# Performance work log

Measured on AMD Instinct MI355X. Metric: run time of the kernel, lower is better.

Reference implementation:

```python
import jax, jax.numpy as jnp
import numpy as np


def _cell(x, h, c, Wih, Whh, bih, bhh):
    # PyTorch LSTM cell, gate order i, f, g, o
    g = x @ Wih.T + h @ Whh.T + bih + bhh
    i, f, gg, o = jnp.split(g, 4, axis=-1)
    c = jax.nn.sigmoid(f) * c + jax.nn.sigmoid(i) * jnp.tanh(gg)
    h = jax.nn.sigmoid(o) * jnp.tanh(c)
    return h, c


def _run_layer(x, Wih, Whh, bih, bhh):
    # x: (B, T, I) -> (hs (B,T,H), hT (B,H), cT (B,H))
    B = x.shape[0]
    H = Whh.shape[1]
    h0 = jnp.zeros((B, H), x.dtype)
    c0 = jnp.zeros((B, H), x.dtype)

    def step(carry, xt):
        h, c = carry
        h, c = _cell(xt, h, c, Wih, Whh, bih, bhh)
        return (h, c), h

    (hT, cT), hs = jax.lax.scan(step, (h0, c0), jnp.swapaxes(x, 0, 1))
    return jnp.swapaxes(hs, 0, 1), hT, cT


def setup_inputs() -> dict:
    key = jax.random.key(0)
    B, T_HIST, F, H, T_FUT = 16384, 20, 10, 128, 30
    s = 0.08  # ~1/sqrt(hidden) init scale
    ks = jax.random.split(key, 20)
    inp = {
        'hist':   jax.random.normal(ks[0], (B, T_HIST, F), jnp.float32),
        'e_Wih0': jax.random.normal(ks[1], (4 * H, F), jnp.float32) * s,
        'e_Whh0': jax.random.normal(ks[2], (4 * H, H), jnp.float32) * s,
        'e_bih0': jax.random.normal(ks[3], (4 * H,), jnp.float32) * s,
        'e_bhh0': jax.random.normal(ks[4], (4 * H,), jnp.float32) * s,
        'e_Wih1': jax.random.normal(ks[5], (4 * H, H), jnp.float32) * s,
        'e_Whh1': jax.random.normal(ks[6], (4 * H, H), jnp.float32) * s,
        'e_bih1': jax.random.normal(ks[7], (4 * H,), jnp.float32) * s,
        'e_bhh1': jax.random.normal(ks[8], (4 * H,), jnp.float32) * s,
        'd_Wih0': jax.random.normal(ks[9], (4 * H, 2), jnp.float32) * s,
        'd_Whh0': jax.random.normal(ks[10], (4 * H, H), jnp.float32) * s,
        'd_bih0': jax.random.normal(ks[11], (4 * H,), jnp.float32) * s,
        'd_bhh0': jax.random.normal(ks[12], (4 * H,), jnp.float32) * s,
        'd_Wih1': jax.random.normal(ks[13], (4 * H, H), jnp.float32) * s,
        'd_Whh1': jax.random.normal(ks[14], (4 * H, H), jnp.float32) * s,
        'd_bih1': jax.random.normal(ks[15], (4 * H,), jnp.float32) * s,
        'd_bhh1': jax.random.normal(ks[16], (4 * H,), jnp.float32) * s,
        'head_W': jax.random.normal(ks[17], (2, H), jnp.float32) * s,
        'head_b': jax.random.normal(ks[18], (2,), jnp.float32) * s,
        'fut_len': T_FUT,
    }
    return inp


def reference(hist, e_Wih0, e_Whh0, e_bih0, e_bhh0, e_Wih1, e_Whh1, e_bih1, e_bhh1,
              d_Wih0, d_Whh0, d_bih0, d_bhh0, d_Wih1, d_Whh1, d_bih1, d_bhh1,
              head_W, head_b, fut_len):
    B = hist.shape[0]
    # 2-layer encoder over history
    h1, hT0, cT0 = _run_layer(hist, e_Wih0, e_Whh0, e_bih0, e_bhh0)
    _, hT1, cT1 = _run_layer(h1, e_Wih1, e_Whh1, e_bih1, e_bhh1)

    def step(carry, _):
        y, h0, c0, h1_, c1_ = carry
        nh0, nc0 = _cell(y, h0, c0, d_Wih0, d_Whh0, d_bih0, d_bhh0)
        nh1, nc1 = _cell(nh0, h1_, c1_, d_Wih1, d_Whh1, d_bih1, d_bhh1)
        dxy = nh1 @ head_W.T + head_b  # (B, 2)
        return (dxy, nh0, nc0, nh1, nc1), dxy

    y0 = jnp.zeros((B, 2), hist.dtype)
    _, ys = jax.lax.scan(step, (y0, hT0, cT0, hT1, cT1), None, length=fut_len)
    return jnp.swapaxes(ys, 0, 1)  # (B, fut_len, 2)
```

## Files before the change

### kernel.cpp

```cpp
#include <hip/hip_runtime.h>


typedef __attribute__((ext_vector_type(8))) short short8;
typedef __attribute__((ext_vector_type(4))) float float4v;

#define MFMA16(a, b, c) __builtin_amdgcn_mfma_f32_16x16x32_bf16((a), (b), (c), 0, 0, 0)

__device__ __forceinline__ unsigned short f2bf(float x) {
    unsigned u = __builtin_bit_cast(unsigned, x);
    unsigned r = (u + 0x7FFFu + ((u >> 16) & 1u)) >> 16;
    return (unsigned short)r;
}
__device__ __forceinline__ float bf2f(unsigned short b) {
    unsigned u = ((unsigned)b) << 16;
    return __builtin_bit_cast(float, u);
}

#if __has_builtin(__builtin_amdgcn_exp2f)
__device__ __forceinline__ float vexp2(float x) { return __builtin_amdgcn_exp2f(x); }
#else
__device__ __forceinline__ float vexp2(float x) { return exp2f(x); }
#endif
#if __has_builtin(__builtin_amdgcn_rcpf)
__device__ __forceinline__ float vrcp(float x) { return __builtin_amdgcn_rcpf(x); }
#else
__device__ __forceinline__ float vrcp(float x) { return 1.0f / x; }
#endif

__device__ __forceinline__ float sigm(float x) {
    return vrcp(1.0f + vexp2(x * -1.442695040888963f));
}
__device__ __forceinline__ float tanh_(float x) {
    return 1.0f - 2.0f * vrcp(1.0f + vexp2(x * 2.885390081777927f));
}

__global__ void prep_kernel(const float* __restrict__ eWih0, const float* __restrict__ eWhh0,
                            const float* __restrict__ ebih0, const float* __restrict__ ebhh0,
                            const float* __restrict__ eWih1, const float* __restrict__ eWhh1,
                            const float* __restrict__ ebih1, const float* __restrict__ ebhh1,
                            const float* __restrict__ dWih0, const float* __restrict__ dWhh0,
                            const float* __restrict__ dbih0, const float* __restrict__ dbhh0,
                            const float* __restrict__ dWih1, const float* __restrict__ dWhh1,
                            const float* __restrict__ dbih1, const float* __restrict__ dbhh1,
                            void* __restrict__ ws)
{
    int i = blockIdx.x * 256 + threadIdx.x;
    short* We0 = (short*)ws;
    short* We1 = We0 + 512 * 160;
    short* Wd0 = We1 + 512 * 256;
    short* Wd1 = Wd0 + 512 * 128;
    float* bsT = (float*)((char*)ws + 819200);
    float* wyT = bsT + 2048;
    const int N0 = 512 * 160, N1 = 512 * 256, N2 = 512 * 128, N3 = 512 * 256;
    if (i < N0) {
        int n = i / 160, k = i - n * 160;
        float v = (k < 32) ? (k < 10 ? eWih0[n * 10 + k] : 0.0f) : eWhh0[n * 128 + (k - 32)];
        We0[i] = (short)f2bf(v);
    } else if (i < N0 + N1) {
        int ii = i - N0, n = ii >> 8, k = ii & 255;
        float v = (k < 128) ? eWih1[n * 128 + k] : eWhh1[n * 128 + (k - 128)];
        We1[ii] = (short)f2bf(v);
    } else if (i < N0 + N1 + N2) {
        int ii = i - (N0 + N1);
        Wd0[ii] = (short)f2bf(dWhh0[ii]);
    } else if (i < N0 + N1 + N2 + N3) {
        int ii = i - (N0 + N1 + N2), n = ii >> 8, k = ii & 255;
        float v = (k < 128) ? dWih1[n * 128 + k] : dWhh1[n * 128 + (k - 128)];
        Wd1[ii] = (short)f2bf(v);
    } else if (i < N0 + N1 + N2 + N3 + 2048) {
        int ii = i - (N0 + N1 + N2 + N3);
        int set = ii >> 9, r = ii & 511, j = r >> 2, q = r & 3;
        int g = q * 128 + j;
        float v = (set == 0) ? ebih0[g] + ebhh0[g]
                : (set == 1) ? ebih1[g] + ebhh1[g]
                : (set == 2) ? dbih0[g] + dbhh0[g]
                             : dbih1[g] + dbhh1[g];
        bsT[ii] = v;
    } else if (i < N0 + N1 + N2 + N3 + 2048 + 1024) {
        int ii = i - (N0 + N1 + N2 + N3 + 2048);
        int j = ii >> 3, e = ii & 7, q = e >> 1, cc = e & 1;
        wyT[ii] = dWih0[(q * 128 + j) * 2 + cc];
    }
}


template <int NKT>
__device__ __forceinline__ void mma4(float4v acc[4][4], const short8* __restrict__ hb,
                                     const char* __restrict__ wb, const unsigned* wo,
                                     int woff, int nib, int quad)
{
#pragma unroll 1
    for (int kk = 0; kk < NKT; ++kk) {
        int sx = ((kk * 4 + quad) ^ nib) + nib * 16;
        short8 a0 = hb[sx];
        short8 a1 = hb[256 + sx];
        short8 a2 = hb[512 + sx];
        short8 a3 = hb[768 + sx];
        short8 b0 = *(const short8*)(wb + (wo[0] + woff + kk * 64));
        short8 b1 = *(const short8*)(wb + (wo[1] + woff + kk * 64));
        short8 b2 = *(const short8*)(wb + (wo[2] + woff + kk * 64));
        short8 b3 = *(const short8*)(wb + (wo[3] + woff + kk * 64));
        acc[0][0] = MFMA16(a0, b0, acc[0][0]);
        acc[0][1] = MFMA16(a1, b0, acc[0][1]);
        acc[0][2] = MFMA16(a2, b0, acc[0][2]);
        acc[0][3] = MFMA16(a3, b0, acc[0][3]);
        acc[1][0] = MFMA16(a0, b1, acc[1][0]);
        acc[1][1] = MFMA16(a1, b1, acc[1][1]);
        acc[1][2] = MFMA16(a2, b1, acc[1][2]);
        acc[1][3] = MFMA16(a3, b1, acc[1][3]);
        acc[2][0] = MFMA16(a0, b2, acc[2][0]);
        acc[2][1] = MFMA16(a1, b2, acc[2][1]);
        acc[2][2] = MFMA16(a2, b2, acc[2][2]);
        acc[2][3] = MFMA16(a3, b2, acc[2][3]);
        acc[3][0] = MFMA16(a0, b3, acc[3][0]);
        acc[3][1] = MFMA16(a1, b3, acc[3][1]);
        acc[3][2] = MFMA16(a2, b3, acc[3][2]);
        acc[3][3] = MFMA16(a3, b3, acc[3][3]);
    }
}

template <bool DEC0>
__device__ __forceinline__ void cell_update4(float4v acc[4][4], float4v bv,
                                             float* __restrict__ cbase,
                                             unsigned short* __restrict__ hdst,
                                             const float* __restrict__ ybuf,
                                             float4v wy0, float4v wy1,
                                             int j, int quad)
{
    int kc = j >> 3;
    int jl = j & 7;
#pragma unroll
    for (int mt = 0; mt < 4; ++mt) {
#pragma unroll
        for (int r = 0; r < 4; ++r) {
            float gi = acc[0][mt][r] + bv[0];
            float gf = acc[1][mt][r] + bv[1];
            float gg = acc[2][mt][r] + bv[2];
            float go = acc[3][mt][r] + bv[3];
            int m = mt * 16 + quad * 4 + r;
            if (DEC0) {
                float y0 = ybuf[2 * m], y1 = ybuf[2 * m + 1];
                gi += y0 * wy0[0] + y1 * wy0[1];
                gf += y0 * wy0[2] + y1 * wy0[3];
                gg += y0 * wy1[0] + y1 * wy1[1];
                go += y0 * wy1[2] + y1 * wy1[3];
            }
            float si = sigm(gi);
            float sf = sigm(gf);
            float tg = tanh_(gg);
            float so = sigm(go);
            float* cp = cbase + (m * 132 + j);
            float c = sf * (*cp) + si * tg;
            *cp = c;
            float h = so * tanh_(c);
            int slot = m * 16 + (kc ^ (m & 15));
            hdst[slot * 8 + jl] = f2bf(h);
        }
    }
}

__global__ void __attribute__((amdgpu_flat_work_group_size(512, 512), amdgpu_waves_per_eu(2)))
lstm_main(
    const float* __restrict__ hist,
    const float* __restrict__ headW, const float* __restrict__ headB,
    const int* __restrict__ futlen, const void* __restrict__ ws,
    float* __restrict__ out)
{
    __shared__ short8 h0buf[2][1024];
    __shared__ short8 h1buf[2][1024];
    __shared__ short8 xbuf[2][256];
    __shared__ float ybuf[128];
    __shared__ float cbuf0[64 * 132];
    __shared__ float cbuf1[64 * 132];

    const char* wsb = (const char*)ws;
    const char* We0 = wsb;
    const char* We1 = wsb + 512 * 160 * 2;
    const char* Wd0 = We1 + 512 * 256 * 2;
    const char* Wd1 = Wd0 + 512 * 128 * 2;
    const float* bsT = (const float*)(wsb + 819200);
    const float* wyT = bsT + 2048;

    const int tid = threadIdx.x;
    const int w = tid >> 6;
    const int lane = tid & 63;
    const int quad = lane >> 4;
    const int nib = lane & 15;
    const int b0 = blockIdx.x * 64;
    const int TFUT = *futlen;
    const int j = 16 * w + nib;

    h0buf[0][tid] = (short8)0;
    h0buf[0][512 + tid] = (short8)0;
    h1buf[0][tid] = (short8)0;
    h1buf[0][512 + tid] = (short8)0;
    h1buf[1][tid] = (short8)0;
    h1buf[1][512 + tid] = (short8)0;
    ((short8*)xbuf)[tid] = (short8)0;
    if (tid < 128) ybuf[tid] = 0.0f;
    for (int i = tid; i < 64 * 132; i += 512) {
        cbuf0[i] = 0.0f;
        cbuf1[i] = 0.0f;
    }
    __syncthreads();

    if (tid < 128) {
        int m = tid & 63, part = tid >> 6;
        const float* hp = hist + ((size_t)((b0 + m) * 20 + 0)) * 10;
        float v[8];
        if (part == 0) {
#pragma unroll
            for (int i = 0; i < 8; ++i) v[i] = hp[i];
        } else {
            v[0] = hp[8]; v[1] = hp[9];
#pragma unroll
            for (int i = 2; i < 8; ++i) v[i] = 0.0f;
        }
        short8 pk;
#pragma unroll
        for (int i = 0; i < 8; ++i) pk[i] = (short)f2bf(v[i]);
        xbuf[0][m * 4 + (part ^ (m & 3))] = pk;
    }

    unsigned eo0[4], eo1[4];
#pragma unroll
    for (int q = 0; q < 4; ++q) {
        unsigned row = 16u * (w + 8 * q) + nib;
        eo0[q] = row * 320u + quad * 16u;
        eo1[q] = row * 512u + quad * 16u;
    }
    int p0 = 0, p1 = 0, px = 0;
    __syncthreads();

#pragma unroll 1
    for (int wdw = 0; wdw < 21; ++wdw) {
        if (wdw < 20) {
            float4v acc[4][4];
#pragma unroll
            for (int q = 0; q < 4; ++q)
#pragma unroll
                for (int mt = 0; mt < 4; ++mt) acc[q][mt] = (float4v){0.f, 0.f, 0.f, 0.f};
            {
                const short8* xb = xbuf[px];
                int sxx = (quad ^ (nib & 3)) + nib * 4;
                short8 a0 = xb[sxx];
                short8 a1 = xb[64 + sxx];
                short8 a2 = xb[128 + sxx];
                short8 a3 = xb[192 + sxx];
                short8 bq0 = *(const short8*)(We0 + eo0[0]);
                short8 bq1 = *(const short8*)(We0 + eo0[1]);
                short8 bq2 = *(const short8*)(We0 + eo0[2]);
                short8 bq3 = *(const short8*)(We0 + eo0[3]);
                acc[0][0] = MFMA16(a0, bq0, acc[0][0]);
                acc[0][1] = MFMA16(a1, bq0, acc[0][1]);
                acc[0][2] = MFMA16(a2, bq0, acc[0][2]);
                acc[0][3] = MFMA16(a3, bq0, acc[0][3]);
                acc[1][0] = MFMA16(a0, bq1, acc[1][0]);
                acc[1][1] = MFMA16(a1, bq1, acc[1][1]);
                acc[1][2] = MFMA16(a2, bq1, acc[1][2]);
                acc[1][3] = MFMA16(a3, bq1, acc[1][3]);
                acc[2][0] = MFMA16(a0, bq2, acc[2][0]);
                acc[2][1] = MFMA16(a1, bq2, acc[2][1]);
                acc[2][2] = MFMA16(a2, bq2, acc[2][2]);
                acc[2][3] = MFMA16(a3, bq2, acc[2][3]);
                acc[3][0] = MFMA16(a0, bq3, acc[3][0]);
                acc[3][1] = MFMA16(a1, bq3, acc[3][1]);
                acc[3][2] = MFMA16(a2, bq3, acc[3][2]);
                acc[3][3] = MFMA16(a3, bq3, acc[3][3]);
            }
            mma4<4>(acc, h0buf[p0], We0, eo0, 64, nib, quad);
            float4v bv = *(const float4v*)(bsT + 0 * 512 + j * 4);
            cell_update4<false>(acc, bv, cbuf0, (unsigned short*)h0buf[p0 ^ 1], nullptr,
                                (float4v){0, 0, 0, 0}, (float4v){0, 0, 0, 0}, j, quad);
        }

        if (tid < 128 && wdw < 19) {
            int m = tid & 63, part = tid >> 6;
            const float* hp = hist + ((size_t)((b0 + m) * 20 + (wdw + 1))) * 10;
            float v[8];
            if (part == 0) {
#pragma unroll
                for (int i = 0; i < 8; ++i) v[i] = hp[i];
            } else {
                v[0] = hp[8]; v[1] = hp[9];
#pragma unroll
                for (int i = 2; i < 8; ++i) v[i] = 0.0f;
            }
            short8 pk;
#pragma unroll
            for (int i = 0; i < 8; ++i) pk[i] = (short)f2bf(v[i]);
            xbuf[px ^ 1][m * 4 + (part ^ (m & 3))] = pk;
        }

        if (wdw >= 1) {
            float4v acc[4][4];
#pragma unroll
            for (int q = 0; q < 4; ++q)
#pragma unroll
                for (int mt = 0; mt < 4; ++mt) acc[q][mt] = (float4v){0.f, 0.f, 0.f, 0.f};
            mma4<4>(acc, h0buf[p0], We1, eo1, 0, nib, quad);
            mma4<4>(acc, h1buf[p1], We1, eo1, 256, nib, quad);
            float4v bv = *(const float4v*)(bsT + 1 * 512 + j * 4);
            cell_update4<false>(acc, bv, cbuf1, (unsigned short*)h1buf[p1 ^ 1], nullptr,
                                (float4v){0, 0, 0, 0}, (float4v){0, 0, 0, 0}, j, quad);
        }
        __syncthreads();
        p0 ^= 1; p1 ^= 1; px ^= 1;
    }

    p0 = 0;
    p1 = 1;

    unsigned do0[4];
#pragma unroll
    for (int q = 0; q < 4; ++q) {
        unsigned row = 16u * (w + 8 * q) + nib;
        do0[q] = row * 256u + quad * 16u;
    }

#pragma unroll 1
    for (int t = 0; t < TFUT; ++t) {
        if (tid < 128 && t >= 1) {
            int m = tid & 63, jj = tid >> 6;
            const short8* hb = h1buf[p1];
            const float4v* hw = (const float4v*)(headW + jj * 128);
            float dot = headB[jj];
            int mk = m & 15;
#pragma unroll
            for (int kc = 0; kc < 16; ++kc) {
                short8 ch = hb[m * 16 + (kc ^ mk)];
                float4v w0 = hw[kc * 2], w1 = hw[kc * 2 + 1];
                dot += bf2f((unsigned short)ch[0]) * w0[0];
                dot += bf2f((unsigned short)ch[1]) * w0[1];
                dot += bf2f((unsigned short)ch[2]) * w0[2];
                dot += bf2f((unsigned short)ch[3]) * w0[3];
                dot += bf2f((unsigned short)ch[4]) * w1[0];
                dot += bf2f((unsigned short)ch[5]) * w1[1];
                dot += bf2f((unsigned short)ch[6]) * w1[2];
                dot += bf2f((unsigned short)ch[7]) * w1[3];
            }
            ybuf[2 * m + jj] = dot;
            out[((size_t)(b0 + m) * TFUT + (t - 1)) * 2 + jj] = dot;
        }

        {
            float4v acc[4][4];
#pragma unroll
            for (int q = 0; q < 4; ++q)
#pragma unroll
                for (int mt = 0; mt < 4; ++mt) acc[q][mt] = (float4v){0.f, 0.f, 0.f, 0.f};
            mma4<4>(acc, h0buf[p0], Wd0, do0, 0, nib, quad);
            float4v bv = *(const float4v*)(bsT + 2 * 512 + j * 4);
            float4v wy0 = *(const float4v*)(wyT + j * 8);
            float4v wy1 = *(const float4v*)(wyT + j * 8 + 4);
            __syncthreads();
            cell_update4<true>(acc, bv, cbuf0, (unsigned short*)h0buf[p0 ^ 1],
                               ybuf, wy0, wy1, j, quad);
        }
        __syncthreads();

        {
            float4v acc[4][4];
#pragma unroll
            for (int q = 0; q < 4; ++q)
#pragma unroll
                for (int mt = 0; mt < 4; ++mt) acc[q][mt] = (float4v){0.f, 0.f, 0.f, 0.f};
            mma4<4>(acc, h0buf[p0 ^ 1], Wd1, eo1, 0, nib, quad);
            mma4<4>(acc, h1buf[p1], Wd1, eo1, 256, nib, quad);
            float4v bv = *(const float4v*)(bsT + 3 * 512 + j * 4);
            cell_update4<false>(acc, bv, cbuf1, (unsigned short*)h1buf[p1 ^ 1], nullptr,
                                (float4v){0, 0, 0, 0}, (float4v){0, 0, 0, 0}, j, quad);
        }
        __syncthreads();
        p0 ^= 1; p1 ^= 1;
    }

    if (tid < 128) {
        int m = tid & 63, jj = tid >> 6;
        const short8* hb = h1buf[p1];
        const float4v* hw = (const float4v*)(headW + jj * 128);
        float dot = headB[jj];
        int mk = m & 15;
#pragma unroll
        for (int kc = 0; kc < 16; ++kc) {
            short8 ch = hb[m * 16 + (kc ^ mk)];
            float4v w0 = hw[kc * 2], w1 = hw[kc * 2 + 1];
            dot += bf2f((unsigned short)ch[0]) * w0[0];
            dot += bf2f((unsigned short)ch[1]) * w0[1];
            dot += bf2f((unsigned short)ch[2]) * w0[2];
            dot += bf2f((unsigned short)ch[3]) * w0[3];
            dot += bf2f((unsigned short)ch[4]) * w1[0];
            dot += bf2f((unsigned short)ch[5]) * w1[1];
            dot += bf2f((unsigned short)ch[6]) * w1[2];
            dot += bf2f((unsigned short)ch[7]) * w1[3];
        }
        out[((size_t)(b0 + m) * TFUT + (TFUT - 1)) * 2 + jj] = dot;
    }
}

extern "C" void kernel_launch(void* const* d_in, const int* in_sizes, int n_in,
                              void* d_out, int out_size, void* d_ws, size_t ws_size,
                              hipStream_t stream)
{
    const float* hist   = (const float*)d_in[0];
    const float* eWih0  = (const float*)d_in[1];
    const float* eWhh0  = (const float*)d_in[2];
    const float* ebih0  = (const float*)d_in[3];
    const float* ebhh0  = (const float*)d_in[4];
    const float* eWih1  = (const float*)d_in[5];
    const float* eWhh1  = (const float*)d_in[6];
    const float* ebih1  = (const float*)d_in[7];
    const float* ebhh1  = (const float*)d_in[8];
    const float* dWih0  = (const float*)d_in[9];
    const float* dWhh0  = (const float*)d_in[10];
    const float* dbih0  = (const float*)d_in[11];
    const float* dbhh0  = (const float*)d_in[12];
    const float* dWih1  = (const float*)d_in[13];
    const float* dWhh1  = (const float*)d_in[14];
    const float* dbih1  = (const float*)d_in[15];
    const float* dbhh1  = (const float*)d_in[16];
    const float* headW  = (const float*)d_in[17];
    const float* headB  = (const float*)d_in[18];
    const int*   futlen = (const int*)d_in[19];

    prep_kernel<<<1612, 256, 0, stream>>>(eWih0, eWhh0, ebih0, ebhh0,
                                          eWih1, eWhh1, ebih1, ebhh1,
                                          dWih0, dWhh0, dbih0, dbhh0,
                                          dWih1, dWhh1, dbih1, dbhh1, d_ws);

    lstm_main<<<256, 512, 0, stream>>>(hist, headW, headB, futlen,
                                       d_ws, (float*)d_out);
}
```

Baseline: 880.7 us.

## Fold output head into decoder layer-0 weights and parallelize head dot product

Precomputes dWih0·headW as extra K columns of the decoder layer-0 weight matrix, and folds dWih0·headB into its bias. This lets the decoder feed back h1 directly through the MFMA instead of waiting on a scalar head dot product. That removes the serial ybuf dependency and one barrier per step. The head output is now computed by all 512 threads as partial sums reduced through shared memory, and the MFMA K-loop start is rotated per block to spread weight-fetch traffic. In exchange it adds 4 extra MFMA K-tiles per decoder step, and the folded weights are rounded to bf16, which changes numerics slightly.

```diff
diff --git a/kernel.cpp b/kernel.cpp
--- a/kernel.cpp
+++ b/kernel.cpp
@@ -42,16 +42,16 @@
                             const float* __restrict__ dbih0, const float* __restrict__ dbhh0,
                             const float* __restrict__ dWih1, const float* __restrict__ dWhh1,
                             const float* __restrict__ dbih1, const float* __restrict__ dbhh1,
+                            const float* __restrict__ headW, const float* __restrict__ headB,
                             void* __restrict__ ws)
 {
     int i = blockIdx.x * 256 + threadIdx.x;
-    short* We0 = (short*)ws;
-    short* We1 = We0 + 512 * 160;
-    short* Wd0 = We1 + 512 * 256;
-    short* Wd1 = Wd0 + 512 * 128;
-    float* bsT = (float*)((char*)ws + 819200);
-    float* wyT = bsT + 2048;
-    const int N0 = 512 * 160, N1 = 512 * 256, N2 = 512 * 128, N3 = 512 * 256;
+    short* We0  = (short*)ws;
+    short* We1  = We0 + 512 * 160;
+    short* Wd0c = We1 + 512 * 256;
+    short* Wd1  = Wd0c + 512 * 256;
+    float* bsT  = (float*)((char*)ws + 950272);
+    const int N0 = 512 * 160, N1 = 512 * 256, N2 = 512 * 256, N3 = 512 * 256;
     if (i < N0) {
         int n = i / 160, k = i - n * 160;
         float v = (k < 32) ? (k < 10 ? eWih0[n * 10 + k] : 0.0f) : eWhh0[n * 128 + (k - 32)];
@@ -61,8 +61,11 @@
         float v = (k < 128) ? eWih1[n * 128 + k] : eWhh1[n * 128 + (k - 128)];
         We1[ii] = (short)f2bf(v);
     } else if (i < N0 + N1 + N2) {
-        int ii = i - (N0 + N1);
-        Wd0[ii] = (short)f2bf(dWhh0[ii]);
+        int ii = i - (N0 + N1), n = ii >> 8, k = ii & 255;
+        float v = (k < 128) ? dWhh0[n * 128 + k]
+                : dWih0[n * 2 + 0] * headW[(k - 128)]
+                + dWih0[n * 2 + 1] * headW[128 + (k - 128)];
+        Wd0c[ii] = (short)f2bf(v);
     } else if (i < N0 + N1 + N2 + N3) {
         int ii = i - (N0 + N1 + N2), n = ii >> 8, k = ii & 255;
         float v = (k < 128) ? dWih1[n * 128 + k] : dWhh1[n * 128 + (k - 128)];
@@ -71,15 +74,14 @@
         int ii = i - (N0 + N1 + N2 + N3);
         int set = ii >> 9, r = ii & 511, j = r >> 2, q = r & 3;
         int g = q * 128 + j;
-        float v = (set == 0) ? ebih0[g] + ebhh0[g]
-                : (set == 1) ? ebih1[g] + ebhh1[g]
-                : (set == 2) ? dbih0[g] + dbhh0[g]
-                             : dbih1[g] + dbhh1[g];
+        float v;
+        if (set == 0)      v = ebih0[g] + ebhh0[g];
+        else if (set == 1) v = ebih1[g] + ebhh1[g];
+        else if (set == 2) v = dbih0[g] + dbhh0[g]
+                             + dWih0[g * 2 + 0] * headB[0]
+                             + dWih0[g * 2 + 1] * headB[1];
+        else               v = dbih1[g] + dbhh1[g];
         bsT[ii] = v;
-    } else if (i < N0 + N1 + N2 + N3 + 2048 + 1024) {
-        int ii = i - (N0 + N1 + N2 + N3 + 2048);
-        int j = ii >> 3, e = ii & 7, q = e >> 1, cc = e & 1;
-        wyT[ii] = dWih0[(q * 128 + j) * 2 + cc];
     }
 }
 
@@ -87,10 +89,11 @@
 template <int NKT>
 __device__ __forceinline__ void mma4(float4v acc[4][4], const short8* __restrict__ hb,
                                      const char* __restrict__ wb, const unsigned* wo,
-                                     int woff, int nib, int quad)
+                                     int woff, int nib, int quad, int rot)
 {
 #pragma unroll 1
-    for (int kk = 0; kk < NKT; ++kk) {
+    for (int kk0 = 0; kk0 < NKT; ++kk0) {
+        int kk = (kk0 + rot) & (NKT - 1);
         int sx = ((kk * 4 + quad) ^ nib) + nib * 16;
         short8 a0 = hb[sx];
         short8 a1 = hb[256 + sx];
@@ -119,12 +122,9 @@
     }
 }
 
-template <bool DEC0>
 __device__ __forceinline__ void cell_update4(float4v acc[4][4], float4v bv,
                                              float* __restrict__ cbase,
                                              unsigned short* __restrict__ hdst,
-                                             const float* __restrict__ ybuf,
-                                             float4v wy0, float4v wy1,
                                              int j, int quad)
 {
     int kc = j >> 3;
@@ -138,13 +138,6 @@
             float gg = acc[2][mt][r] + bv[2];
             float go = acc[3][mt][r] + bv[3];
             int m = mt * 16 + quad * 4 + r;
-            if (DEC0) {
-                float y0 = ybuf[2 * m], y1 = ybuf[2 * m + 1];
-                gi += y0 * wy0[0] + y1 * wy0[1];
-                gf += y0 * wy0[2] + y1 * wy0[3];
-                gg += y0 * wy1[0] + y1 * wy1[1];
-                go += y0 * wy1[2] + y1 * wy1[3];
-            }
             float si = sigm(gi);
             float sf = sigm(gf);
             float tg = tanh_(gg);
@@ -169,17 +162,16 @@
     __shared__ short8 h0buf[2][1024];
     __shared__ short8 h1buf[2][1024];
     __shared__ short8 xbuf[2][256];
-    __shared__ float ybuf[128];
+    __shared__ float hpart[512];
     __shared__ float cbuf0[64 * 132];
     __shared__ float cbuf1[64 * 132];
 
-    const char* wsb = (const char*)ws;
-    const char* We0 = wsb;
-    const char* We1 = wsb + 512 * 160 * 2;
-    const char* Wd0 = We1 + 512 * 256 * 2;
-    const char* Wd1 = Wd0 + 512 * 128 * 2;
-    const float* bsT = (const float*)(wsb + 819200);
-    const float* wyT = bsT + 2048;
+    const char* wsb  = (const char*)ws;
+    const char* We0  = wsb;
+    const char* We1  = wsb + 163840;
+    const char* Wd0c = wsb + 425984;
+    const char* Wd1  = wsb + 688128;
+    const float* bsT = (const float*)(wsb + 950272);
 
     const int tid = threadIdx.x;
     const int w = tid >> 6;
@@ -189,6 +181,7 @@
     const int b0 = blockIdx.x * 64;
     const int TFUT = *futlen;
     const int j = 16 * w + nib;
+    const int rotk = blockIdx.x & 3;
 
     h0buf[0][tid] = (short8)0;
     h0buf[0][512 + tid] = (short8)0;
@@ -197,7 +190,6 @@
     h1buf[1][tid] = (short8)0;
     h1buf[1][512 + tid] = (short8)0;
     ((short8*)xbuf)[tid] = (short8)0;
-    if (tid < 128) ybuf[tid] = 0.0f;
     for (int i = tid; i < 64 * 132; i += 512) {
         cbuf0[i] = 0.0f;
         cbuf1[i] = 0.0f;
@@ -268,10 +260,9 @@
                 acc[3][2] = MFMA16(a2, bq3, acc[3][2]);
                 acc[3][3] = MFMA16(a3, bq3, acc[3][3]);
             }
-            mma4<4>(acc, h0buf[p0], We0, eo0, 64, nib, quad);
+            mma4<4>(acc, h0buf[p0], We0, eo0, 64, nib, quad, rotk);
             float4v bv = *(const float4v*)(bsT + 0 * 512 + j * 4);
-            cell_update4<false>(acc, bv, cbuf0, (unsigned short*)h0buf[p0 ^ 1], nullptr,
-                                (float4v){0, 0, 0, 0}, (float4v){0, 0, 0, 0}, j, quad);
+            cell_update4(acc, bv, cbuf0, (unsigned short*)h0buf[p0 ^ 1], j, quad);
         }
 
         if (tid < 128 && wdw < 19) {
@@ -298,11 +289,10 @@
             for (int q = 0; q < 4; ++q)
 #pragma unroll
                 for (int mt = 0; mt < 4; ++mt) acc[q][mt] = (float4v){0.f, 0.f, 0.f, 0.f};
-            mma4<4>(acc, h0buf[p0], We1, eo1, 0, nib, quad);
-            mma4<4>(acc, h1buf[p1], We1, eo1, 256, nib, quad);
+            mma4<4>(acc, h0buf[p0], We1, eo1, 0, nib, quad, rotk);
+            mma4<4>(acc, h1buf[p1], We1, eo1, 256, nib, quad, rotk);
             float4v bv = *(const float4v*)(bsT + 1 * 512 + j * 4);
-            cell_update4<false>(acc, bv, cbuf1, (unsigned short*)h1buf[p1 ^ 1], nullptr,
-                                (float4v){0, 0, 0, 0}, (float4v){0, 0, 0, 0}, j, quad);
+            cell_update4(acc, bv, cbuf1, (unsigned short*)h1buf[p1 ^ 1], j, quad);
         }
         __syncthreads();
         p0 ^= 1; p1 ^= 1; px ^= 1;
@@ -311,23 +301,18 @@
     p0 = 0;
     p1 = 1;
 
-    unsigned do0[4];
-#pragma unroll
-    for (int q = 0; q < 4; ++q) {
-        unsigned row = 16u * (w + 8 * q) + nib;
-        do0[q] = row * 256u + quad * 16u;
-    }
-
 #pragma unroll 1
     for (int t = 0; t < TFUT; ++t) {
-        if (tid < 128 && t >= 1) {
-            int m = tid & 63, jj = tid >> 6;
+        if (t >= 1) {
+            int pair = tid >> 2, qh = tid & 3;
+            int m = pair >> 1, jj = pair & 1;
             const short8* hb = h1buf[p1];
             const float4v* hw = (const float4v*)(headW + jj * 128);
-            float dot = headB[jj];
             int mk = m & 15;
-#pragma unroll
-            for (int kc = 0; kc < 16; ++kc) {
+            float dot = 0.0f;
+#pragma unroll
+            for (int kq = 0; kq < 4; ++kq) {
+                int kc = qh * 4 + kq;
                 short8 ch = hb[m * 16 + (kc ^ mk)];
                 float4v w0 = hw[kc * 2], w1 = hw[kc * 2 + 1];
                 dot += bf2f((unsigned short)ch[0]) * w0[0];
@@ -339,8 +324,7 @@
                 dot += bf2f((unsigned short)ch[6]) * w1[2];
                 dot += bf2f((unsigned short)ch[7]) * w1[3];
             }
-            ybuf[2 * m + jj] = dot;
-            out[((size_t)(b0 + m) * TFUT + (t - 1)) * 2 + jj] = dot;
+            hpart[tid] = dot;
         }
 
         {
@@ -349,15 +333,20 @@
             for (int q = 0; q < 4; ++q)
 #pragma unroll
                 for (int mt = 0; mt < 4; ++mt) acc[q][mt] = (float4v){0.f, 0.f, 0.f, 0.f};
-            mma4<4>(acc, h0buf[p0], Wd0, do0, 0, nib, quad);
+            mma4<4>(acc, h0buf[p0], Wd0c, eo1, 0, nib, quad, rotk);
+            if (t > 0)
+                mma4<4>(acc, h1buf[p1], Wd0c, eo1, 256, nib, quad, rotk);
             float4v bv = *(const float4v*)(bsT + 2 * 512 + j * 4);
-            float4v wy0 = *(const float4v*)(wyT + j * 8);
-            float4v wy1 = *(const float4v*)(wyT + j * 8 + 4);
-            __syncthreads();
-            cell_update4<true>(acc, bv, cbuf0, (unsigned short*)h0buf[p0 ^ 1],
-                               ybuf, wy0, wy1, j, quad);
+            cell_update4(acc, bv, cbuf0, (unsigned short*)h0buf[p0 ^ 1], j, quad);
         }
         __syncthreads();
+
+        if (tid < 128 && t >= 1) {
+            int m = tid >> 1, jj = tid & 1;
+            float dot = headB[jj] + hpart[tid * 4] + hpart[tid * 4 + 1]
+                      + hpart[tid * 4 + 2] + hpart[tid * 4 + 3];
+            out[((size_t)(b0 + m) * TFUT + (t - 1)) * 2 + jj] = dot;
+        }
 
         {
             float4v acc[4][4];
@@ -365,24 +354,25 @@
             for (int q = 0; q < 4; ++q)
 #pragma unroll
                 for (int mt = 0; mt < 4; ++mt) acc[q][mt] = (float4v){0.f, 0.f, 0.f, 0.f};
-            mma4<4>(acc, h0buf[p0 ^ 1], Wd1, eo1, 0, nib, quad);
-            mma4<4>(acc, h1buf[p1], Wd1, eo1, 256, nib, quad);
+            mma4<4>(acc, h0buf[p0 ^ 1], Wd1, eo1, 0, nib, quad, rotk);
+            mma4<4>(acc, h1buf[p1], Wd1, eo1, 256, nib, quad, rotk);
             float4v bv = *(const float4v*)(bsT + 3 * 512 + j * 4);
-            cell_update4<false>(acc, bv, cbuf1, (unsigned short*)h1buf[p1 ^ 1], nullptr,
-                                (float4v){0, 0, 0, 0}, (float4v){0, 0, 0, 0}, j, quad);
+            cell_update4(acc, bv, cbuf1, (unsigned short*)h1buf[p1 ^ 1], j, quad);
         }
         __syncthreads();
         p0 ^= 1; p1 ^= 1;
     }
 
-    if (tid < 128) {
-        int m = tid & 63, jj = tid >> 6;
+    {
+        int pair = tid >> 2, qh = tid & 3;
+        int m = pair >> 1, jj = pair & 1;
         const short8* hb = h1buf[p1];
         const float4v* hw = (const float4v*)(headW + jj * 128);
-        float dot = headB[jj];
         int mk = m & 15;
-#pragma unroll
-        for (int kc = 0; kc < 16; ++kc) {
+        float dot = 0.0f;
+#pragma unroll
+        for (int kq = 0; kq < 4; ++kq) {
+            int kc = qh * 4 + kq;
             short8 ch = hb[m * 16 + (kc ^ mk)];
             float4v w0 = hw[kc * 2], w1 = hw[kc * 2 + 1];
             dot += bf2f((unsigned short)ch[0]) * w0[0];
@@ -394,6 +384,13 @@
             dot += bf2f((unsigned short)ch[6]) * w1[2];
             dot += bf2f((unsigned short)ch[7]) * w1[3];
         }
+        hpart[tid] = dot;
+    }
+    __syncthreads();
+    if (tid < 128) {
+        int m = tid >> 1, jj = tid & 1;
+        float dot = headB[jj] + hpart[tid * 4] + hpart[tid * 4 + 1]
+                  + hpart[tid * 4 + 2] + hpart[tid * 4 + 3];
         out[((size_t)(b0 + m) * TFUT + (TFUT - 1)) * 2 + jj] = dot;
     }
 }
@@ -423,10 +420,11 @@
     const float* headB  = (const float*)d_in[18];
     const int*   futlen = (const int*)d_in[19];
 
-    prep_kernel<<<1612, 256, 0, stream>>>(eWih0, eWhh0, ebih0, ebhh0,
+    prep_kernel<<<1864, 256, 0, stream>>>(eWih0, eWhh0, ebih0, ebhh0,
                                           eWih1, eWhh1, ebih1, ebhh1,
                                           dWih0, dWhh0, dbih0, dbhh0,
-                                          dWih1, dWhh1, dbih1, dbhh1, d_ws);
+                                          dWih1, dWhh1, dbih1, dbhh1,
+                                          headW, headB, d_ws);
 
     lstm_main<<<256, 512, 0, stream>>>(hist, headW, headB, futlen,
                                        d_ws, (float*)d_out);
```

After: 979.3 us. 1.11x slower.
